# Optimization experiments

Measured on AMD Instinct MI355X. Metric: run time of the kernel, lower is better.

Reference implementation:

```python
import jax, jax.numpy as jnp
import numpy as np

B, S, D = 2, 2048, 1024
H, HD = 16, 64

def setup_inputs() -> dict:
    key = jax.random.key(0)
    ks = jax.random.split(key, 5)
    scale = 1.0 / np.sqrt(D)
    x = jax.random.normal(ks[0], (B, S, D), dtype=jnp.float32)
    wq = jax.random.normal(ks[1], (D, H * HD), dtype=jnp.float32) * scale
    wk = jax.random.normal(ks[2], (D, H * HD), dtype=jnp.float32) * scale
    wv = jax.random.normal(ks[3], (D, H * HD), dtype=jnp.float32) * scale
    wo = jax.random.normal(ks[4], (H * HD, D), dtype=jnp.float32) * scale
    zeros = jnp.zeros((H * HD,), dtype=jnp.float32)
    return {"x": x, "wq": wq, "bq": zeros, "wk": wk, "bk": zeros,
            "wv": wv, "bv": zeros, "wo": wo, "bo": jnp.zeros((D,), jnp.float32)}

def reference(x, wq, bq, wk, bk, wv, bv, wo, bo):
    b, s, _ = x.shape
    att_scale = HD ** -0.5
    # QKV projections -> [b, h, s, hd]
    q = (x @ wq + bq).reshape(b, s, H, HD).transpose(0, 2, 1, 3)
    k = (x @ wk + bk).reshape(b, s, H, HD).transpose(0, 2, 1, 3)
    v = (x @ wv + bv).reshape(b, s, H, HD).transpose(0, 2, 1, 3)
    scores = jnp.einsum('bhqd,bhkd->bhqk', q, k) * att_scale
    weights = jax.nn.softmax(scores, axis=-1)
    out = jnp.einsum('bhqk,bhkd->bhqd', weights, v)
    out = out.transpose(0, 2, 1, 3).reshape(b, s, H * HD)
    return out @ wo + bo
```

## Files before the change

kernel.cpp:

```cpp
#include <hip/hip_runtime.h>
#include <hip/hip_bf16.h>

#define B_  2
#define S_  2048
#define D_  1024
#define H_  16
#define HD_ 64
#define M_  (B_*S_)

using bf16x8 = __attribute__((ext_vector_type(8))) short;
using f32x4  = __attribute__((ext_vector_type(4))) float;
using f32x16 = __attribute__((ext_vector_type(16))) float;
using u32x4  = __attribute__((ext_vector_type(4))) unsigned int;
using uint2v = __attribute__((ext_vector_type(2))) unsigned int;

static __device__ __forceinline__ ushort f2bf(float f) {
    __hip_bfloat16 h = __float2bfloat16(f);
    return *reinterpret_cast<ushort*>(&h);
}
static __device__ __forceinline__ float max3f(float a, float b, float c) {
    return fmaxf(fmaxf(a, b), c);
}
static __device__ __forceinline__ float fexp2(float x) {
#if __has_builtin(__builtin_amdgcn_exp2f)
    return __builtin_amdgcn_exp2f(x);
#else
    return exp2f(x);
#endif
}
static __device__ __forceinline__ unsigned int pack_bf16(float p0, float p1) {
    unsigned int a = __float_as_uint(p0), b = __float_as_uint(p1);
    a += 0x7fffu + ((a >> 16) & 1u);
    b += 0x7fffu + ((b >> 16) & 1u);
    return (a >> 16) | (b & 0xffff0000u);
}

#define GLDS16(gp, lp) __builtin_amdgcn_global_load_lds( \
    (const __attribute__((address_space(1))) void*)(gp), \
    (__attribute__((address_space(3))) void*)(lp), 16, 0, 0)

__global__ void prep(const float* __restrict__ x,
                     const float* __restrict__ wq, const float* __restrict__ wk,
                     const float* __restrict__ wv, const float* __restrict__ wo,
                     ushort* __restrict__ xb, ushort* __restrict__ wqkvT, ushort* __restrict__ woT) {
    const int z = blockIdx.z;
    if (z == 4) {
        int blk = blockIdx.y * 32 + blockIdx.x;
        int tid = threadIdx.y * 32 + threadIdx.x;
        #pragma unroll
        for (int q = 0; q < 4; q++) {
            int i = ((q * 1024 + blk) * 256 + tid) * 4;
            float4 v = *reinterpret_cast<const float4*>(x + i);
            ushort4 o;
            o.x = f2bf(v.x); o.y = f2bf(v.y); o.z = f2bf(v.z); o.w = f2bf(v.w);
            *reinterpret_cast<ushort4*>(xb + i) = o;
        }
        return;
    }
    const float* src = (z == 0) ? wq : (z == 1) ? wk : (z == 2) ? wv : wo;
    ushort* dst = (z < 3) ? (wqkvT + (size_t)z * 1024 * 1024) : woT;
    const int R = 1024, C = 1024;
    __shared__ float t[32][33];
    int c0 = blockIdx.x * 32, r0 = blockIdx.y * 32;
    int tx = threadIdx.x, ty = threadIdx.y;
    #pragma unroll
    for (int i = 0; i < 4; i++)
        t[ty + i*8][tx] = src[(size_t)(r0 + ty + i*8) * C + c0 + tx];
    __syncthreads();
    #pragma unroll
    for (int i = 0; i < 4; i++)
        dst[(size_t)(c0 + ty + i*8) * R + r0 + tx] = f2bf(t[tx][ty + i*8]);
}

template<int MODE, int NJ>
__launch_bounds__(256, 3)
__global__ void gemm_bt(const ushort* __restrict__ A, const ushort* __restrict__ Bt,
                        int Mdim, int Ndim, int Kdim,
                        ushort* __restrict__ qout, ushort* __restrict__ kout, ushort* __restrict__ vout,
                        const float* __restrict__ bq, const float* __restrict__ bk, const float* __restrict__ bv,
                        float* __restrict__ out, const float* __restrict__ bias)
{
    constexpr int BN = NJ * 32;
    __shared__ __align__(16) ushort As[128][64];
    __shared__ __align__(16) ushort Bs[BN][64];
    const int tid  = threadIdx.x;
    const int lane = tid & 63, wave = tid >> 6;
    const int wm = wave & 1, wn = wave >> 1;
    const int lin = blockIdx.x;
    const int xcd = lin & 7, idx = lin >> 3;
    int my, nx;
    if (MODE == 0) { my = (xcd >> 1) * 8 + idx / 12; nx = (xcd & 1) * 12 + idx % 12; }
    else           { my = xcd * 4 + (idx >> 4);      nx = idx & 15; }
    const int m0 = my * 128, n0 = nx * BN;
    const int g = lane >> 4, c = lane & 15;

    f32x4 acc[4][NJ];
    #pragma unroll
    for (int i = 0; i < 4; i++)
        #pragma unroll
        for (int j = 0; j < NJ; j++) acc[i][j] = (f32x4){0.f, 0.f, 0.f, 0.f};

    const int arow  = lane >> 3;
    const int aslot = (lane & 7) ^ arow;
    const ushort* Ag = A  + (size_t)(m0 + arow) * Kdim + aslot * 8;
    const ushort* Bg = Bt + (size_t)(n0 + arow) * Kdim + aslot * 8;

    #pragma unroll 1
    for (int kt = 0; kt < Kdim; kt += 64) {
        #pragma unroll
        for (int p = 0; p < 4; p++) {
            int ch = wave + p * 4;
            GLDS16(Ag + (size_t)(ch*8) * Kdim + kt, &As[ch*8][0]);
        }
        #pragma unroll
        for (int p = 0; p < NJ; p++) {
            int ch = wave + p * 4;
            GLDS16(Bg + (size_t)(ch*8) * Kdim + kt, &Bs[ch*8][0]);
        }
        __syncthreads();
        #pragma unroll
        for (int ks = 0; ks < 2; ks++) {
            bf16x8 af[4], bfr[NJ];
            #pragma unroll
            for (int t = 0; t < 4; t++) {
                int sl = ((ks*4 + g) ^ (c & 7)) * 8;
                af[t] = *reinterpret_cast<const bf16x8*>(&As[wm*64 + t*16 + c][sl]);
            }
            #pragma unroll
            for (int t = 0; t < NJ; t++) {
                int sl = ((ks*4 + g) ^ (c & 7)) * 8;
                bfr[t] = *reinterpret_cast<const bf16x8*>(&Bs[wn*(NJ*16) + t*16 + c][sl]);
            }
            #pragma unroll
            for (int i = 0; i < 4; i++)
                #pragma unroll
                for (int j = 0; j < NJ; j++)
                    acc[i][j] = __builtin_amdgcn_mfma_f32_16x16x32_bf16(af[i], bfr[j], acc[i][j], 0, 0, 0);
        }
        __syncthreads();
    }

    const float qscale = 0.125f * 1.4426950408889634f;
    if (MODE == 0) {
        const int which = n0 >> 10;
        const int cc0 = (n0 & 1023) + wn*64;
        const int h = cc0 >> 6;
        const int b = m0 >> 11;
        if (which == 2) {
            float bj[4];
            #pragma unroll
            for (int j = 0; j < 4; j++) bj[j] = bv[cc0 + j*16 + c];
            const int sbase = (m0 & 2047) + wm*64 + g*4;
            ushort* vb = vout + (size_t)(b*H_ + h) * HD_ * S_;
            #pragma unroll
            for (int i = 0; i < 4; i++) {
                int s0 = sbase + i*16;
                #pragma unroll
                for (int j = 0; j < 4; j++) {
                    int hd = j*16 + c;
                    ushort4 o;
                    o.x = f2bf(acc[i][j][0] + bj[j]);
                    o.y = f2bf(acc[i][j][1] + bj[j]);
                    o.z = f2bf(acc[i][j][2] + bj[j]);
                    o.w = f2bf(acc[i][j][3] + bj[j]);
                    *reinterpret_cast<ushort4*>(vb + (size_t)hd * S_ + s0) = o;
                }
            }
        } else {
            ushort* dst0 = (which == 0) ? qout : kout;
            const float* bp = (which == 0) ? bq : bk;
            const float scl = (which == 0) ? qscale : 1.f;
            float bj[4];
            #pragma unroll
            for (int j = 0; j < 4; j++) bj[j] = bp[cc0 + j*16 + c];
            #pragma unroll
            for (int i = 0; i < 4; i++) {
                #pragma unroll
                for (int r = 0; r < 4; r++) {
                    int row = m0 + wm*64 + i*16 + g*4 + r;
                    int s = row & 2047;
                    ushort* orow = dst0 + (((size_t)(b*H_ + h)) * S_ + s) * HD_;
                    #pragma unroll
                    for (int j = 0; j < 4; j++)
                        orow[j*16 + c] = f2bf((acc[i][j][r] + bj[j]) * scl);
                }
            }
        }
    } else {
        float bj[NJ];
        #pragma unroll
        for (int j = 0; j < NJ; j++) bj[j] = bias[n0 + wn*(NJ*16) + j*16 + c];
        #pragma unroll
        for (int i = 0; i < 4; i++)
            #pragma unroll
            for (int r = 0; r < 4; r++) {
                int row = m0 + wm*64 + i*16 + g*4 + r;
                float* orow = out + (size_t)row * Ndim + n0 + wn*(NJ*16);
                #pragma unroll
                for (int j = 0; j < NJ; j++)
                    orow[j*16 + c] = acc[i][j][r] + bj[j];
            }
    }
}

__launch_bounds__(512, 4)
__global__ void attn_kernel(const ushort* __restrict__ Q, const ushort* __restrict__ K,
                            const ushort* __restrict__ Vt, ushort* __restrict__ O)
{
    __shared__ __align__(16) ushort Ks[2][2][64][64];
    __shared__ __align__(16) ushort Vs[2][2][64][64];
    const int tid = threadIdx.x, lane = tid & 63, w = tid >> 6;
    const int grp = w >> 2, wq4 = w & 3;
    const int q31 = lane & 31, hi = lane >> 5, x7 = lane & 7;

    int lin = blockIdx.x + gridDim.x * blockIdx.y;
    int xcd = lin & 7, idx = lin >> 3;
    int bh = xcd * 4 + (idx & 3);
    int qb = idx >> 2;
    const int q0 = qb * 128;
    const int kt_base = grp * 1024;
    const ushort* Kp = K  + (size_t)bh * S_ * HD_;
    const ushort* Vp = Vt + (size_t)bh * HD_ * S_;

    bf16x8 qf[4];
    #pragma unroll
    for (int c4 = 0; c4 < 4; c4++)
        qf[c4] = *reinterpret_cast<const bf16x8*>(
            Q + (size_t)bh * S_ * HD_ + (size_t)(q0 + wq4*32 + q31) * HD_ + c4*16 + hi*8);

    f32x16 acc0, acc1;
    #pragma unroll
    for (int r = 0; r < 16; r++) { acc0[r] = 0.f; acc1[r] = 0.f; }
    float m_i = -INFINITY, l_i = 0.f;

    const int srow  = lane >> 3;
    const int sslot = (lane & 7) ^ srow;
    const ushort* kg = Kp + (size_t)srow * HD_ + sslot * 8;
    const ushort* vg = Vp + (size_t)srow * S_  + sslot * 8;

    auto stage = [&](int buf, int kt) {
        #pragma unroll
        for (int p = 0; p < 2; p++) {
            int ch = wq4 + p * 4;
            GLDS16(kg + (size_t)(kt + ch*8) * HD_, &Ks[grp][buf][ch*8][0]);
            GLDS16(vg + (size_t)(ch*8) * S_ + kt,  &Vs[grp][buf][ch*8][0]);
        }
    };

    auto softmax_pack = [&](const f32x16& st, bf16x8& pf0, bf16x8& pf1) {
        float g0 = max3f(st[0],  st[1],  st[2]);
        float g1 = max3f(st[3],  st[4],  st[5]);
        float g2 = max3f(st[6],  st[7],  st[8]);
        float g3 = max3f(st[9],  st[10], st[11]);
        float g4 = max3f(st[12], st[13], st[14]);
        float pm = fmaxf(max3f(g0, g1, g2), max3f(g3, g4, st[15]));
#if __has_builtin(__builtin_amdgcn_permlane32_swap)
        {
            uint2v r = __builtin_amdgcn_permlane32_swap(__float_as_uint(pm), __float_as_uint(pm), false, false);
            pm = fmaxf(__uint_as_float(r.x), __uint_as_float(r.y));
        }
#else
        pm = fmaxf(pm, __shfl_xor(pm, 32));
#endif
        if (__any(pm > m_i + 8.f)) {
            float mnew = fmaxf(m_i, pm);
            float al = fexp2(m_i - mnew);
            l_i *= al;
            #pragma unroll
            for (int r = 0; r < 16; r++) { acc0[r] *= al; acc1[r] *= al; }
            m_i = mnew;
        }
        float rs = 0.f;
        unsigned int dd[8];
        #pragma unroll
        for (int r2 = 0; r2 < 8; r2++) {
            float p0 = fexp2(st[r2*2]     - m_i);
            float p1 = fexp2(st[r2*2 + 1] - m_i);
            rs += p0 + p1;
            dd[r2] = pack_bf16(p0, p1);
        }
#if __has_builtin(__builtin_amdgcn_permlane32_swap)
        {
            uint2v r = __builtin_amdgcn_permlane32_swap(__float_as_uint(rs), __float_as_uint(rs), false, false);
            rs = __uint_as_float(r.x) + __uint_as_float(r.y);
        }
#else
        rs += __shfl_xor(rs, 32);
#endif
        l_i += rs;
        u32x4 t0, t1;
#if __has_builtin(__builtin_amdgcn_permlane32_swap)
        {
            uint2v s02 = __builtin_amdgcn_permlane32_swap(dd[0], dd[2], false, false);
            uint2v s13 = __builtin_amdgcn_permlane32_swap(dd[1], dd[3], false, false);
            uint2v s46 = __builtin_amdgcn_permlane32_swap(dd[4], dd[6], false, false);
            uint2v s57 = __builtin_amdgcn_permlane32_swap(dd[5], dd[7], false, false);
            t0 = (u32x4){s02.x, s13.x, s02.y, s13.y};
            t1 = (u32x4){s46.x, s57.x, s46.y, s57.y};
        }
#else
        {
            unsigned int ee[8];
            #pragma unroll
            for (int r2 = 0; r2 < 8; r2++)
                ee[r2] = (unsigned int)__shfl_xor((int)dd[r2], 32);
            t0 = (u32x4){ hi ? ee[2] : dd[0], hi ? ee[3] : dd[1],
                          hi ? dd[2] : ee[0], hi ? dd[3] : ee[1] };
            t1 = (u32x4){ hi ? ee[6] : dd[4], hi ? ee[7] : dd[5],
                          hi ? dd[6] : ee[4], hi ? dd[7] : ee[5] };
        }
#endif
        pf0 = *reinterpret_cast<bf16x8*>(&t0);
        pf1 = *reinterpret_cast<bf16x8*>(&t1);
    };

    auto compute64 = [&](int buf) {
        const ushort (*ks)[64] = Ks[grp][buf];
        const ushort (*vs)[64] = Vs[grp][buf];
        f32x16 st0, st1;
        #pragma unroll
        for (int r = 0; r < 16; r++) { st0[r] = 0.f; st1[r] = 0.f; }
        __builtin_amdgcn_s_setprio(1);
        #pragma unroll
        for (int c4 = 0; c4 < 4; c4++) {
            bf16x8 kf = *reinterpret_cast<const bf16x8*>(&ks[q31][((c4*2 + hi) ^ x7) * 8]);
            st0 = __builtin_amdgcn_mfma_f32_32x32x16_bf16(kf, qf[c4], st0, 0, 0, 0);
        }
        #pragma unroll
        for (int c4 = 0; c4 < 4; c4++) {
            bf16x8 kf = *reinterpret_cast<const bf16x8*>(&ks[32 + q31][((c4*2 + hi) ^ x7) * 8]);
            st1 = __builtin_amdgcn_mfma_f32_32x32x16_bf16(kf, qf[c4], st1, 0, 0, 0);
        }
        __builtin_amdgcn_s_setprio(0);

        bf16x8 pf0, pf1;
        softmax_pack(st0, pf0, pf1);
        {
            bf16x8 vf0 = *reinterpret_cast<const bf16x8*>(&vs[q31]     [((0 + hi) ^ x7) * 8]);
            bf16x8 vf1 = *reinterpret_cast<const bf16x8*>(&vs[q31]     [((2 + hi) ^ x7) * 8]);
            bf16x8 vf2 = *reinterpret_cast<const bf16x8*>(&vs[32 + q31][((0 + hi) ^ x7) * 8]);
            bf16x8 vf3 = *reinterpret_cast<const bf16x8*>(&vs[32 + q31][((2 + hi) ^ x7) * 8]);
            __builtin_amdgcn_s_setprio(1);
            acc0 = __builtin_amdgcn_mfma_f32_32x32x16_bf16(vf0, pf0, acc0, 0, 0, 0);
            acc0 = __builtin_amdgcn_mfma_f32_32x32x16_bf16(vf1, pf1, acc0, 0, 0, 0);
            acc1 = __builtin_amdgcn_mfma_f32_32x32x16_bf16(vf2, pf0, acc1, 0, 0, 0);
            acc1 = __builtin_amdgcn_mfma_f32_32x32x16_bf16(vf3, pf1, acc1, 0, 0, 0);
            __builtin_amdgcn_s_setprio(0);
        }
        softmax_pack(st1, pf0, pf1);
        {
            bf16x8 vf0 = *reinterpret_cast<const bf16x8*>(&vs[q31]     [((4 + hi) ^ x7) * 8]);
            bf16x8 vf1 = *reinterpret_cast<const bf16x8*>(&vs[q31]     [((6 + hi) ^ x7) * 8]);
            bf16x8 vf2 = *reinterpret_cast<const bf16x8*>(&vs[32 + q31][((4 + hi) ^ x7) * 8]);
            bf16x8 vf3 = *reinterpret_cast<const bf16x8*>(&vs[32 + q31][((6 + hi) ^ x7) * 8]);
            __builtin_amdgcn_s_setprio(1);
            acc0 = __builtin_amdgcn_mfma_f32_32x32x16_bf16(vf0, pf0, acc0, 0, 0, 0);
            acc0 = __builtin_amdgcn_mfma_f32_32x32x16_bf16(vf1, pf1, acc0, 0, 0, 0);
            acc1 = __builtin_amdgcn_mfma_f32_32x32x16_bf16(vf2, pf0, acc1, 0, 0, 0);
            acc1 = __builtin_amdgcn_mfma_f32_32x32x16_bf16(vf3, pf1, acc1, 0, 0, 0);
            __builtin_amdgcn_s_setprio(0);
        }
    };

    stage(0, kt_base);
    __syncthreads();
    #pragma unroll 1
    for (int it = 0; it < 15; ++it) {
        stage((it & 1) ^ 1, kt_base + (it + 1) * 64);
        compute64(it & 1);
        __syncthreads();
    }
    compute64(1);

    __syncthreads();
    float* fb = (wq4 < 2) ? reinterpret_cast<float*>(&Ks[0][0][0][0])
                          : reinterpret_cast<float*>(&Vs[0][0][0][0]);
    const int slot = ((wq4 & 1) * 64 + lane) * 35;
    if (grp == 1) {
        #pragma unroll
        for (int r = 0; r < 16; r++) { fb[slot + r] = acc0[r]; fb[slot + 16 + r] = acc1[r]; }
        fb[slot + 32] = m_i;
        fb[slot + 33] = l_i;
    }
    __syncthreads();
    if (grp == 0) {
        float m2 = fb[slot + 32], l2 = fb[slot + 33];
        float mm = fmaxf(m_i, m2);
        float a1 = fexp2(m_i - mm), a2 = fexp2(m2 - mm);
        float inv = 1.f / (l_i * a1 + l2 * a2);
        const int b = bh >> 4, h = bh & 15;
        const int s = q0 + wq4*32 + q31;
        ushort* op = O + (size_t)(b*S_ + s) * 1024 + h*64;
        #pragma unroll
        for (int rg = 0; rg < 4; rg++) {
            int hd0 = rg*8 + hi*4;
            ushort4 o;
            o.x = f2bf((acc0[rg*4+0]*a1 + fb[slot + rg*4+0]*a2) * inv);
            o.y = f2bf((acc0[rg*4+1]*a1 + fb[slot + rg*4+1]*a2) * inv);
            o.z = f2bf((acc0[rg*4+2]*a1 + fb[slot + rg*4+2]*a2) * inv);
            o.w = f2bf((acc0[rg*4+3]*a1 + fb[slot + rg*4+3]*a2) * inv);
            *reinterpret_cast<ushort4*>(op + hd0) = o;
            o.x = f2bf((acc1[rg*4+0]*a1 + fb[slot + 16 + rg*4+0]*a2) * inv);
            o.y = f2bf((acc1[rg*4+1]*a1 + fb[slot + 16 + rg*4+1]*a2) * inv);
            o.z = f2bf((acc1[rg*4+2]*a1 + fb[slot + 16 + rg*4+2]*a2) * inv);
            o.w = f2bf((acc1[rg*4+3]*a1 + fb[slot + 16 + rg*4+3]*a2) * inv);
            *reinterpret_cast<ushort4*>(op + 32 + hd0) = o;
        }
    }
}

extern "C" void kernel_launch(void* const* d_in, const int* in_sizes, int n_in,
                              void* d_out, int out_size, void* d_ws, size_t ws_size,
                              hipStream_t stream)
{
    const float* x  = (const float*)d_in[0];
    const float* wq = (const float*)d_in[1];
    const float* bq = (const float*)d_in[2];
    const float* wk = (const float*)d_in[3];
    const float* bk = (const float*)d_in[4];
    const float* wv = (const float*)d_in[5];
    const float* bv = (const float*)d_in[6];
    const float* wo = (const float*)d_in[7];
    const float* bo = (const float*)d_in[8];
    float* out = (float*)d_out;

    char* ws = (char*)d_ws;
    ushort* xb    = (ushort*)(ws);
    ushort* wqkvT = (ushort*)(ws + (8ull  << 20));
    ushort* woT   = (ushort*)(ws + (14ull << 20));
    ushort* qw    = (ushort*)(ws + (16ull << 20));
    ushort* kw    = (ushort*)(ws + (24ull << 20));
    ushort* vtw   = (ushort*)(ws + (32ull << 20));
    ushort* ao    = (ushort*)(ws + (40ull << 20));

    prep<<<dim3(32, 32, 5), dim3(32, 8), 0, stream>>>(x, wq, wk, wv, wo, xb, wqkvT, woT);

    gemm_bt<0, 4><<<768, 256, 0, stream>>>(xb, wqkvT, M_, 3072, 1024,
                                           qw, kw, vtw, bq, bk, bv, nullptr, nullptr);
    attn_kernel<<<dim3(16, 32), 512, 0, stream>>>(qw, kw, vtw, ao);
    gemm_bt<1, 2><<<512, 256, 0, stream>>>(ao, woT, M_, 1024, 1024,
                                           nullptr, nullptr, nullptr, nullptr, nullptr, nullptr,
                                           out, bo);
}
```

Baseline: 193.1 us.

## Double-buffer GEMM LDS tiles with 32-wide K steps to overlap loads and MFMA

The projection GEMM now keeps two 32-wide K slices in shared memory and issues the global-to-LDS loads for the next slice before computing the current one. This hides global load latency behind MFMA work and cuts the barriers to one per iteration instead of two. In exchange there are twice as many loop iterations, and the LDS swizzle is changed to fit the 32-element rows. Shared memory use stays the same.

```diff
diff --git a/kernel.cpp b/kernel.cpp
--- a/kernel.cpp
+++ b/kernel.cpp
@@ -81,8 +81,8 @@
                         float* __restrict__ out, const float* __restrict__ bias)
 {
     constexpr int BN = NJ * 32;
-    __shared__ __align__(16) ushort As[128][64];
-    __shared__ __align__(16) ushort Bs[BN][64];
+    __shared__ __align__(16) ushort As[2][128][32];
+    __shared__ __align__(16) ushort Bs[2][BN][32];
     const int tid  = threadIdx.x;
     const int lane = tid & 63, wave = tid >> 6;
     const int wm = wave & 1, wn = wave >> 1;
@@ -100,45 +100,50 @@
         #pragma unroll
         for (int j = 0; j < NJ; j++) acc[i][j] = (f32x4){0.f, 0.f, 0.f, 0.f};
 
-    const int arow  = lane >> 3;
-    const int aslot = (lane & 7) ^ arow;
+    const int arow  = lane >> 2;
+    const int aslot = (lane & 3) ^ ((lane >> 3) & 3);
     const ushort* Ag = A  + (size_t)(m0 + arow) * Kdim + aslot * 8;
     const ushort* Bg = Bt + (size_t)(n0 + arow) * Kdim + aslot * 8;
 
+    auto stage = [&](int buf, int kt) {
+        #pragma unroll
+        for (int p = 0; p < 2; p++) {
+            int ch = wave + p * 4;
+            GLDS16(Ag + (size_t)(ch*16) * Kdim + kt, &As[buf][ch*16][0]);
+        }
+        #pragma unroll
+        for (int p = 0; p < NJ/2; p++) {
+            int ch = wave + p * 4;
+            GLDS16(Bg + (size_t)(ch*16) * Kdim + kt, &Bs[buf][ch*16][0]);
+        }
+    };
+
+    auto compute = [&](int buf) {
+        bf16x8 af[4], bfr[NJ];
+        const int sl = (g ^ ((c >> 1) & 3)) * 8;
+        #pragma unroll
+        for (int t = 0; t < 4; t++)
+            af[t] = *reinterpret_cast<const bf16x8*>(&As[buf][wm*64 + t*16 + c][sl]);
+        #pragma unroll
+        for (int t = 0; t < NJ; t++)
+            bfr[t] = *reinterpret_cast<const bf16x8*>(&Bs[buf][wn*(NJ*16) + t*16 + c][sl]);
+        #pragma unroll
+        for (int i = 0; i < 4; i++)
+            #pragma unroll
+            for (int j = 0; j < NJ; j++)
+                acc[i][j] = __builtin_amdgcn_mfma_f32_16x16x32_bf16(af[i], bfr[j], acc[i][j], 0, 0, 0);
+    };
+
+    const int NT = Kdim >> 5;
+    stage(0, 0);
+    __syncthreads();
     #pragma unroll 1
-    for (int kt = 0; kt < Kdim; kt += 64) {
-        #pragma unroll
-        for (int p = 0; p < 4; p++) {
-            int ch = wave + p * 4;
-            GLDS16(Ag + (size_t)(ch*8) * Kdim + kt, &As[ch*8][0]);
-        }
-        #pragma unroll
-        for (int p = 0; p < NJ; p++) {
-            int ch = wave + p * 4;
-            GLDS16(Bg + (size_t)(ch*8) * Kdim + kt, &Bs[ch*8][0]);
-        }
+    for (int it = 0; it < NT - 1; ++it) {
+        stage((it + 1) & 1, (it + 1) * 32);
+        compute(it & 1);
         __syncthreads();
-        #pragma unroll
-        for (int ks = 0; ks < 2; ks++) {
-            bf16x8 af[4], bfr[NJ];
-            #pragma unroll
-            for (int t = 0; t < 4; t++) {
-                int sl = ((ks*4 + g) ^ (c & 7)) * 8;
-                af[t] = *reinterpret_cast<const bf16x8*>(&As[wm*64 + t*16 + c][sl]);
-            }
-            #pragma unroll
-            for (int t = 0; t < NJ; t++) {
-                int sl = ((ks*4 + g) ^ (c & 7)) * 8;
-                bfr[t] = *reinterpret_cast<const bf16x8*>(&Bs[wn*(NJ*16) + t*16 + c][sl]);
-            }
-            #pragma unroll
-            for (int i = 0; i < 4; i++)
-                #pragma unroll
-                for (int j = 0; j < NJ; j++)
-                    acc[i][j] = __builtin_amdgcn_mfma_f32_16x16x32_bf16(af[i], bfr[j], acc[i][j], 0, 0, 0);
-        }
-        __syncthreads();
-    }
+    }
+    compute((NT - 1) & 1);
 
     const float qscale = 0.125f * 1.4426950408889634f;
     if (MODE == 0) {
```

Result: slower. 198.1 us (+2.6%).

## Add dedicated double-buffered 512-thread QKV GEMM kernel

Applied to the files above, without the earlier changes.

Replaces the templated QKV projection GEMM with a dedicated kernel that uses 8 waves per 128x128 tile and double-buffered shared memory. The next K-slice is loaded into LDS while the current one is computed, which needs one barrier per iteration instead of two. Each wave now owns a 64x32 sub-tile, so it holds fewer accumulators per thread and more waves are resident. The cost is twice the LDS per block (64KB), which may limit occupancy, and the wider grid adds more per-block overhead.

```diff
diff --git a/kernel.cpp b/kernel.cpp
--- a/kernel.cpp
+++ b/kernel.cpp
@@ -72,12 +72,122 @@
         dst[(size_t)(c0 + ty + i*8) * R + r0 + tx] = f2bf(t[tx][ty + i*8]);
 }
 
+__launch_bounds__(512, 4)
+__global__ void gemm_qkv(const ushort* __restrict__ A, const ushort* __restrict__ Bt,
+                         ushort* __restrict__ qout, ushort* __restrict__ kout, ushort* __restrict__ vout,
+                         const float* __restrict__ bq, const float* __restrict__ bk, const float* __restrict__ bv)
+{
+    const int Kdim = 1024;
+    __shared__ __align__(16) ushort As[2][128][64];
+    __shared__ __align__(16) ushort Bs[2][128][64];
+    const int tid  = threadIdx.x;
+    const int lane = tid & 63, wave = tid >> 6;
+    const int wm = wave & 1, wn = wave >> 1;
+    const int lin = blockIdx.x;
+    const int xcd = lin & 7, idx = lin >> 3;
+    const int my = (xcd >> 1) * 8 + idx / 12, nx = (xcd & 1) * 12 + idx % 12;
+    const int m0 = my * 128, n0 = nx * 128;
+    const int g = lane >> 4, c = lane & 15;
+
+    f32x4 acc[4][2];
+    #pragma unroll
+    for (int i = 0; i < 4; i++)
+        #pragma unroll
+        for (int j = 0; j < 2; j++) acc[i][j] = (f32x4){0.f, 0.f, 0.f, 0.f};
+
+    const int arow  = lane >> 3;
+    const int aslot = (lane & 7) ^ arow;
+    const ushort* Ag = A  + (size_t)(m0 + arow) * Kdim + aslot * 8;
+    const ushort* Bg = Bt + (size_t)(n0 + arow) * Kdim + aslot * 8;
+
+    auto stage = [&](int buf, int kt) {
+        GLDS16(Ag + (size_t)(wave*8)       * Kdim + kt, &As[buf][wave*8][0]);
+        GLDS16(Ag + (size_t)((wave+8)*8)   * Kdim + kt, &As[buf][(wave+8)*8][0]);
+        GLDS16(Bg + (size_t)(wave*8)       * Kdim + kt, &Bs[buf][wave*8][0]);
+        GLDS16(Bg + (size_t)((wave+8)*8)   * Kdim + kt, &Bs[buf][(wave+8)*8][0]);
+    };
+
+    auto compute = [&](int buf) {
+        #pragma unroll
+        for (int ks = 0; ks < 2; ks++) {
+            const int sl = ((ks*4 + g) ^ (c & 7)) * 8;
+            bf16x8 af[4], bfr[2];
+            #pragma unroll
+            for (int t = 0; t < 4; t++)
+                af[t] = *reinterpret_cast<const bf16x8*>(&As[buf][wm*64 + t*16 + c][sl]);
+            #pragma unroll
+            for (int t = 0; t < 2; t++)
+                bfr[t] = *reinterpret_cast<const bf16x8*>(&Bs[buf][wn*32 + t*16 + c][sl]);
+            #pragma unroll
+            for (int i = 0; i < 4; i++)
+                #pragma unroll
+                for (int j = 0; j < 2; j++)
+                    acc[i][j] = __builtin_amdgcn_mfma_f32_16x16x32_bf16(af[i], bfr[j], acc[i][j], 0, 0, 0);
+        }
+    };
+
+    stage(0, 0);
+    __syncthreads();
+    #pragma unroll 1
+    for (int it = 0; it < 15; ++it) {
+        stage((it + 1) & 1, (it + 1) * 64);
+        compute(it & 1);
+        __syncthreads();
+    }
+    compute(1);
+
+    const float qscale = 0.125f * 1.4426950408889634f;
+    const int which = n0 >> 10;
+    const int cc0 = (n0 & 1023) + wn*32;
+    const int h = cc0 >> 6;
+    const int hd0 = cc0 & 63;
+    const int b = m0 >> 11;
+    if (which == 2) {
+        float bj[2];
+        #pragma unroll
+        for (int j = 0; j < 2; j++) bj[j] = bv[cc0 + j*16 + c];
+        const int sbase = (m0 & 2047) + wm*64 + g*4;
+        ushort* vb = vout + (size_t)(b*H_ + h) * HD_ * S_;
+        #pragma unroll
+        for (int i = 0; i < 4; i++) {
+            int s0 = sbase + i*16;
+            #pragma unroll
+            for (int j = 0; j < 2; j++) {
+                int hd = hd0 + j*16 + c;
+                ushort4 o;
+                o.x = f2bf(acc[i][j][0] + bj[j]);
+                o.y = f2bf(acc[i][j][1] + bj[j]);
+                o.z = f2bf(acc[i][j][2] + bj[j]);
+                o.w = f2bf(acc[i][j][3] + bj[j]);
+                *reinterpret_cast<ushort4*>(vb + (size_t)hd * S_ + s0) = o;
+            }
+        }
+    } else {
+        ushort* dst0 = (which == 0) ? qout : kout;
+        const float* bp = (which == 0) ? bq : bk;
+        const float scl = (which == 0) ? qscale : 1.f;
+        float bj[2];
+        #pragma unroll
+        for (int j = 0; j < 2; j++) bj[j] = bp[cc0 + j*16 + c];
+        #pragma unroll
+        for (int i = 0; i < 4; i++) {
+            #pragma unroll
+            for (int r = 0; r < 4; r++) {
+                int row = m0 + wm*64 + i*16 + g*4 + r;
+                int s = row & 2047;
+                ushort* orow = dst0 + (((size_t)(b*H_ + h)) * S_ + s) * HD_;
+                #pragma unroll
+                for (int j = 0; j < 2; j++)
+                    orow[hd0 + j*16 + c] = f2bf((acc[i][j][r] + bj[j]) * scl);
+            }
+        }
+    }
+}
+
 template<int MODE, int NJ>
 __launch_bounds__(256, 3)
 __global__ void gemm_bt(const ushort* __restrict__ A, const ushort* __restrict__ Bt,
                         int Mdim, int Ndim, int Kdim,
-                        ushort* __restrict__ qout, ushort* __restrict__ kout, ushort* __restrict__ vout,
-                        const float* __restrict__ bq, const float* __restrict__ bk, const float* __restrict__ bv,
                         float* __restrict__ out, const float* __restrict__ bias)
 {
     constexpr int BN = NJ * 32;
@@ -88,9 +198,7 @@
     const int wm = wave & 1, wn = wave >> 1;
     const int lin = blockIdx.x;
     const int xcd = lin & 7, idx = lin >> 3;
-    int my, nx;
-    if (MODE == 0) { my = (xcd >> 1) * 8 + idx / 12; nx = (xcd & 1) * 12 + idx % 12; }
-    else           { my = xcd * 4 + (idx >> 4);      nx = idx & 15; }
+    const int my = xcd * 4 + (idx >> 4), nx = idx & 15;
     const int m0 = my * 128, n0 = nx * BN;
     const int g = lane >> 4, c = lane & 15;
 
@@ -140,67 +248,19 @@
         __syncthreads();
     }
 
-    const float qscale = 0.125f * 1.4426950408889634f;
-    if (MODE == 0) {
-        const int which = n0 >> 10;
-        const int cc0 = (n0 & 1023) + wn*64;
-        const int h = cc0 >> 6;
-        const int b = m0 >> 11;
-        if (which == 2) {
-            float bj[4];
-            #pragma unroll
-            for (int j = 0; j < 4; j++) bj[j] = bv[cc0 + j*16 + c];
-            const int sbase = (m0 & 2047) + wm*64 + g*4;
-            ushort* vb = vout + (size_t)(b*H_ + h) * HD_ * S_;
-            #pragma unroll
-            for (int i = 0; i < 4; i++) {
-                int s0 = sbase + i*16;
-                #pragma unroll
-                for (int j = 0; j < 4; j++) {
-                    int hd = j*16 + c;
-                    ushort4 o;
-                    o.x = f2bf(acc[i][j][0] + bj[j]);
-                    o.y = f2bf(acc[i][j][1] + bj[j]);
-                    o.z = f2bf(acc[i][j][2] + bj[j]);
-                    o.w = f2bf(acc[i][j][3] + bj[j]);
-                    *reinterpret_cast<ushort4*>(vb + (size_t)hd * S_ + s0) = o;
-                }
-            }
-        } else {
-            ushort* dst0 = (which == 0) ? qout : kout;
-            const float* bp = (which == 0) ? bq : bk;
-            const float scl = (which == 0) ? qscale : 1.f;
-            float bj[4];
-            #pragma unroll
-            for (int j = 0; j < 4; j++) bj[j] = bp[cc0 + j*16 + c];
-            #pragma unroll
-            for (int i = 0; i < 4; i++) {
-                #pragma unroll
-                for (int r = 0; r < 4; r++) {
-                    int row = m0 + wm*64 + i*16 + g*4 + r;
-                    int s = row & 2047;
-                    ushort* orow = dst0 + (((size_t)(b*H_ + h)) * S_ + s) * HD_;
-                    #pragma unroll
-                    for (int j = 0; j < 4; j++)
-                        orow[j*16 + c] = f2bf((acc[i][j][r] + bj[j]) * scl);
-                }
-            }
-        }
-    } else {
-        float bj[NJ];
-        #pragma unroll
-        for (int j = 0; j < NJ; j++) bj[j] = bias[n0 + wn*(NJ*16) + j*16 + c];
-        #pragma unroll
-        for (int i = 0; i < 4; i++)
-            #pragma unroll
-            for (int r = 0; r < 4; r++) {
-                int row = m0 + wm*64 + i*16 + g*4 + r;
-                float* orow = out + (size_t)row * Ndim + n0 + wn*(NJ*16);
-                #pragma unroll
-                for (int j = 0; j < NJ; j++)
-                    orow[j*16 + c] = acc[i][j][r] + bj[j];
-            }
-    }
+    float bj[NJ];
+    #pragma unroll
+    for (int j = 0; j < NJ; j++) bj[j] = bias[n0 + wn*(NJ*16) + j*16 + c];
+    #pragma unroll
+    for (int i = 0; i < 4; i++)
+        #pragma unroll
+        for (int r = 0; r < 4; r++) {
+            int row = m0 + wm*64 + i*16 + g*4 + r;
+            float* orow = out + (size_t)row * Ndim + n0 + wn*(NJ*16);
+            #pragma unroll
+            for (int j = 0; j < NJ; j++)
+                orow[j*16 + c] = acc[i][j][r] + bj[j];
+        }
 }
 
 __launch_bounds__(512, 4)
@@ -435,10 +495,7 @@
 
     prep<<<dim3(32, 32, 5), dim3(32, 8), 0, stream>>>(x, wq, wk, wv, wo, xb, wqkvT, woT);
 
-    gemm_bt<0, 4><<<768, 256, 0, stream>>>(xb, wqkvT, M_, 3072, 1024,
-                                           qw, kw, vtw, bq, bk, bv, nullptr, nullptr);
+    gemm_qkv<<<768, 512, 0, stream>>>(xb, wqkvT, qw, kw, vtw, bq, bk, bv);
     attn_kernel<<<dim3(16, 32), 512, 0, stream>>>(qw, kw, vtw, ao);
-    gemm_bt<1, 2><<<512, 256, 0, stream>>>(ao, woT, M_, 1024, 1024,
-                                           nullptr, nullptr, nullptr, nullptr, nullptr, nullptr,
-                                           out, bo);
-}
+    gemm_bt<1, 2><<<512, 256, 0, stream>>>(ao, woT, M_, 1024, 1024, out, bo);
+}
```

New measurement: 204.9 us. +6.1%, slower.
